# Kernel tuning notes

Measured on AMD Instinct MI355X. Metric: run time of the kernel, lower is better.

Reference implementation:

```python
import jax, jax.numpy as jnp
from jax import lax
import numpy as np

B, S, W = 32, 256, 16
WORD_VOCAB, WORD_DIM = 100000, 300
CHAR_VOCAB, CHAR_DIM = 101, 16  # len(char_vocab)+1
CH, WH = 16, 32                 # char_lstm_dim, lstm_size
GEN = 100
N_LABELS = 2


def _lstm(x, Wih, Whh, b, reverse=False):
    """Single-direction LSTM. x: [T, N, D]. Returns (outputs [T,N,H], final h [N,H]).
    Torch gate order: i, f, g, o."""
    pre = jnp.einsum('tnd,hd->tnh', x, Wih) + b  # [T, N, 4H]
    if reverse:
        pre = pre[::-1]
    H = Whh.shape[1]
    N = x.shape[1]

    def step(carry, xt):
        h, c = carry
        g = xt + h @ Whh.T
        i, f, gg, o = jnp.split(g, 4, axis=-1)
        c = jax.nn.sigmoid(f) * c + jax.nn.sigmoid(i) * jnp.tanh(gg)
        h = jax.nn.sigmoid(o) * jnp.tanh(c)
        return (h, c), h

    init = (jnp.zeros((N, H), x.dtype), jnp.zeros((N, H), x.dtype))
    (hT, _), hs = lax.scan(step, init, pre)
    if reverse:
        hs = hs[::-1]
    return hs, hT


def setup_inputs() -> dict:
    key = jax.random.key(0)
    ks = jax.random.split(key, 16)
    sc = lambda *shape: 0.1

    def rn(k, shape):
        return jax.random.normal(k, shape, dtype=jnp.float32) * 0.1

    return {
        'word_ids': jax.random.randint(ks[0], (B, S), 0, WORD_VOCAB),
        'char_ids': jax.random.randint(ks[1], (B, S, W), 0, CHAR_VOCAB),
        'word_table': rn(ks[2], (WORD_VOCAB, WORD_DIM)),
        'char_table': rn(ks[3], (CHAR_VOCAB, CHAR_DIM)),
        'c_Wih_f': rn(ks[4], (4 * CH, CHAR_DIM)), 'c_Whh_f': rn(ks[5], (4 * CH, CH)),
        'c_b_f': jnp.zeros((4 * CH,), jnp.float32),
        'c_Wih_b': rn(ks[6], (4 * CH, CHAR_DIM)), 'c_Whh_b': rn(ks[7], (4 * CH, CH)),
        'c_b_b': jnp.zeros((4 * CH,), jnp.float32),
        'gen_W': rn(ks[8], (GEN, WORD_DIM + 2 * CH)), 'gen_b': jnp.zeros((GEN,), jnp.float32),
        'w_Wih_f': rn(ks[9], (4 * WH, GEN)), 'w_Whh_f': rn(ks[10], (4 * WH, WH)),
        'w_b_f': jnp.zeros((4 * WH,), jnp.float32),
        'w_Wih_b': rn(ks[11], (4 * WH, GEN)), 'w_Whh_b': rn(ks[12], (4 * WH, WH)),
        'w_b_b': jnp.zeros((4 * WH,), jnp.float32),
        'out_W': rn(ks[13], (N_LABELS, 2 * WH)), 'out_b': jnp.zeros((N_LABELS,), jnp.float32),
    }


def reference(word_ids, char_ids, word_table, char_table,
              c_Wih_f, c_Whh_f, c_b_f, c_Wih_b, c_Whh_b, c_b_b,
              gen_W, gen_b,
              w_Wih_f, w_Whh_f, w_b_f, w_Wih_b, w_Whh_b, w_b_b,
              out_W, out_b):
    # Word embedding lookup: [B, S, WORD_DIM]
    word_e = word_table[word_ids]
    # Char embedding: [B, S, W, CHAR_DIM] -> char biLSTM over W, final states.
    char_e = char_table[char_ids].reshape(B * S, W, CHAR_DIM).transpose(1, 0, 2)  # [W, B*S, C]
    _, hf = _lstm(char_e, c_Wih_f, c_Whh_f, c_b_f, reverse=False)
    _, hb = _lstm(char_e, c_Wih_b, c_Whh_b, c_b_b, reverse=True)
    char_repr = jnp.concatenate([hf, hb], axis=-1).reshape(B, S, 2 * CH)
    # Concat word + char reprs, gen layer + gelu (dropout p=0 / eval).
    word_output = jnp.concatenate([word_e, char_repr], axis=-1)  # [B, S, 332]
    word_vecs = jax.nn.gelu(word_output @ gen_W.T + gen_b, approximate=False)  # [B, S, GEN]
    # Word-level biLSTM over S, per-step outputs.
    x = word_vecs.transpose(1, 0, 2)  # [S, B, GEN]
    of, _ = _lstm(x, w_Wih_f, w_Whh_f, w_b_f, reverse=False)
    ob, _ = _lstm(x, w_Wih_b, w_Whh_b, w_b_b, reverse=True)
    lstm_out = jnp.concatenate([of, ob], axis=-1).transpose(1, 0, 2)  # [B, S, 2*WH]
    # Output layer + sigmoid.
    return jax.nn.sigmoid(lstm_out @ out_W.T + out_b)  # [B, S, N_LABELS]
```

## Files before the change

### kernel.cpp

```cpp
#include <hip/hip_runtime.h>
#include <hip/hip_bf16.h>

#define B_    32
#define S_    256
#define BS_   8192
#define Wc_   16
#define CDIM_ 16
#define CH_   16
#define WDIM_ 300
#define KX_   332
#define XC_   336
#define GEN_  100
#define WVP_  104
#define WH_   32
#define NG_   128

constexpr size_t OFF_WV   = 0;
constexpr size_t OFF_PRE  = OFF_WV   + (size_t)BS_*WVP_;
constexpr size_t OFF_LO   = OFF_PRE  + (size_t)2*S_*B_*NG_;
constexpr size_t OFF_CHB  = OFF_LO   + (size_t)BS_*64;
constexpr size_t OFF_GWT  = OFF_CHB  + (size_t)BS_*32;
constexpr size_t OFF_WIHT = OFF_GWT  + (size_t)KX_*128;
constexpr size_t OFF_WHHT = OFF_WIHT + (size_t)2*GEN_*NG_;
constexpr size_t OFF_OW   = OFF_WHHT + (size_t)2*WH_*NG_;

__device__ __forceinline__ float sigm(float x){ return __builtin_amdgcn_rcpf(1.f + __expf(-x)); }
__device__ __forceinline__ float tanh_(float x){ return 1.f - 2.f*__builtin_amdgcn_rcpf(1.f + __expf(2.f*x)); }
__device__ __forceinline__ float rdlane(float v, int lane){
  return __uint_as_float(__builtin_amdgcn_readlane(__float_as_uint(v), lane));
}

__global__ void k_prep(const float* gen_W, const float* wih_f, const float* wih_b,
                       const float* whh_f, const float* whh_b, const float* out_W,
                       float* ws){
  int idx = blockIdx.x*blockDim.x + threadIdx.x;
  int stride = gridDim.x*blockDim.x;
  for (int i = idx; i < GEN_*KX_; i += stride){
    int j = i / KX_, k = i - j*KX_;
    ws[OFF_GWT + (size_t)k*128 + j] = gen_W[i];
  }
  for (int i = idx; i < NG_*GEN_; i += stride){
    int g = i / GEN_, k = i - g*GEN_;
    ws[OFF_WIHT + 0*GEN_*NG_ + (size_t)k*NG_ + g] = wih_f[i];
    ws[OFF_WIHT + 1*GEN_*NG_ + (size_t)k*NG_ + g] = wih_b[i];
  }
  for (int i = idx; i < NG_*WH_; i += stride){
    int g = i / WH_, k = i - g*WH_;
    ws[OFF_WHHT + 0*WH_*NG_ + (size_t)k*NG_ + g] = whh_f[i];
    ws[OFF_WHHT + 1*WH_*NG_ + (size_t)k*NG_ + g] = whh_b[i];
  }
  for (int i = idx; i < 2*64; i += stride) ws[OFF_OW + i] = out_W[i];
}

__global__ void __launch_bounds__(256, 2) k_char(const int* char_ids, const float* char_table,
                       const float* Wih_f, const float* Whh_f, const float* b_f,
                       const float* Wih_b, const float* Whh_b, const float* b_b,
                       float* ws){
  __shared__ float xr[16*324];
  const int dir = blockIdx.x & 1;
  const int sg  = blockIdx.x >> 1;
  const int tid = threadIdx.x;
  const float* WI = dir ? Wih_b : Wih_f;
  const float* WH = dir ? Whh_b : Whh_f;
  const float* BB = dir ? b_b  : b_f;
  const int ls = tid >> 4, u = tid & 15;
  const int seq0 = sg * 16;
  {
    const int id = char_ids[(seq0 + ls)*Wc_ + u];
    const float4* sr = (const float4*)(char_table + (size_t)id*CDIM_);
    float4 v0 = sr[0], v1 = sr[1], v2 = sr[2], v3 = sr[3];
    float* xw = &xr[ls*324 + u*20];
    *(float4*)(xw+0)  = v0; *(float4*)(xw+4)  = v1;
    *(float4*)(xw+8)  = v2; *(float4*)(xw+12) = v3;
  }
  float wi[4][16];
  #pragma unroll
  for (int g = 0; g < 4; ++g){
    const float4* wr = (const float4*)(WI + (size_t)(g*16+u)*CDIM_);
    float4 a = wr[0], b = wr[1], c = wr[2], d = wr[3];
    wi[g][0]=a.x; wi[g][1]=a.y; wi[g][2]=a.z; wi[g][3]=a.w;
    wi[g][4]=b.x; wi[g][5]=b.y; wi[g][6]=b.z; wi[g][7]=b.w;
    wi[g][8]=c.x; wi[g][9]=c.y; wi[g][10]=c.z; wi[g][11]=c.w;
    wi[g][12]=d.x; wi[g][13]=d.y; wi[g][14]=d.z; wi[g][15]=d.w;
  }
  float bias[4];
  #pragma unroll
  for (int g = 0; g < 4; ++g) bias[g] = BB[g*16+u];
  __syncthreads();
  float xp[16][4];
  const float* xb = &xr[ls*324];
  #pragma unroll
  for (int p = 0; p < 16; ++p){
    const int tm = dir ? (15-p) : p;
    const float4 x0 = *(const float4*)(xb + tm*20 + 0);
    const float4 x1 = *(const float4*)(xb + tm*20 + 4);
    const float4 x2 = *(const float4*)(xb + tm*20 + 8);
    const float4 x3 = *(const float4*)(xb + tm*20 + 12);
    float xk[16] = {x0.x,x0.y,x0.z,x0.w, x1.x,x1.y,x1.z,x1.w,
                    x2.x,x2.y,x2.z,x2.w, x3.x,x3.y,x3.z,x3.w};
    #pragma unroll
    for (int g = 0; g < 4; ++g){
      float a0 = bias[g], a1 = 0.f;
      #pragma unroll
      for (int k = 0; k < 16; k += 2){ a0 += wi[g][k]*xk[k]; a1 += wi[g][k+1]*xk[k+1]; }
      xp[p][g] = a0 + a1;
    }
  }
  float wh[4][16];
  #pragma unroll
  for (int g = 0; g < 4; ++g){
    const float4* wr = (const float4*)(WH + (size_t)(g*16+u)*CH_);
    float4 a = wr[0], b = wr[1], c = wr[2], d = wr[3];
    wh[g][0]=a.x; wh[g][1]=a.y; wh[g][2]=a.z; wh[g][3]=a.w;
    wh[g][4]=b.x; wh[g][5]=b.y; wh[g][6]=b.z; wh[g][7]=b.w;
    wh[g][8]=c.x; wh[g][9]=c.y; wh[g][10]=c.z; wh[g][11]=c.w;
    wh[g][12]=d.x; wh[g][13]=d.y; wh[g][14]=d.z; wh[g][15]=d.w;
  }
  const int lbase = (tid & 63) & 48;
  float h = 0.f, c = 0.f;
  #pragma unroll
  for (int p = 0; p < 16; ++p){
    float ai = xp[p][0], af = xp[p][1], ag = xp[p][2], ao = xp[p][3];
    #pragma unroll
    for (int k = 0; k < 16; ++k){
      const float hk = __shfl(h, lbase + k, 64);
      ai += wh[0][k]*hk; af += wh[1][k]*hk;
      ag += wh[2][k]*hk; ao += wh[3][k]*hk;
    }
    c = sigm(af)*c + sigm(ai)*tanh_(ag);
    h = sigm(ao)*tanh_(c);
  }
  ws[OFF_CHB + (size_t)(seq0 + ls)*32 + dir*16 + u] = h;
}

__global__ void k_gen(const int* word_ids, const float* word_table, const float* gen_b, float* ws){
  __shared__ __align__(16) float xt[16*XC_];
  __shared__ int wids[16];
  const int r0 = blockIdx.x*16;
  if (threadIdx.x < 16) wids[threadIdx.x] = word_ids[r0 + threadIdx.x];
  __syncthreads();
  float4* xt4 = (float4*)xt;
  for (int i = threadIdx.x; i < 16*75; i += 128){
    const int r = i/75, q = i - r*75;
    xt4[r*84 + q] = ((const float4*)(word_table + (size_t)wids[r]*WDIM_))[q];
  }
  for (int i = threadIdx.x; i < 16*8; i += 128){
    const int r = i >> 3, q = i & 7;
    xt4[r*84 + 75 + q] = ((const float4*)(ws + OFF_CHB + (size_t)(r0+r)*32))[q];
  }
  __syncthreads();
  const int j = threadIdx.x;
  const float bj = (j < GEN_) ? gen_b[j] : 0.f;
  float acc[16];
  #pragma unroll
  for (int r = 0; r < 16; ++r) acc[r] = bj;
  const float* WT = ws + OFF_GWT;
  for (int k4 = 0; k4 < KX_/4; ++k4){
    const int k = k4*4;
    const float w0 = WT[(size_t)(k+0)*128 + j];
    const float w1 = WT[(size_t)(k+1)*128 + j];
    const float w2 = WT[(size_t)(k+2)*128 + j];
    const float w3 = WT[(size_t)(k+3)*128 + j];
    #pragma unroll
    for (int r = 0; r < 16; ++r){
      const float4 xv = xt4[r*84 + k4];
      acc[r] += w0*xv.x + w1*xv.y + w2*xv.z + w3*xv.w;
    }
  }
  if (j < GEN_){
    float* wv = ws + OFF_WV;
    #pragma unroll
    for (int r = 0; r < 16; ++r){
      const float a = acc[r];
      wv[(size_t)(r0+r)*WVP_ + j] = 0.5f*a*(1.f + erff(a*0.70710678118f));
    }
  }
}

__global__ void k_wpre(const float* wb_f, const float* wb_b, float* ws){
  __shared__ __align__(16) float xt[8*WVP_];
  const int d  = blockIdx.x & 1;
  const int r0 = (blockIdx.x >> 1)*8;
  const float4* WVr = (const float4*)(ws + OFF_WV + (size_t)r0*WVP_);
  float4* xt4 = (float4*)xt;
  for (int i = threadIdx.x; i < 8*(WVP_/4); i += 128) xt4[i] = WVr[i];
  __syncthreads();
  const int g = threadIdx.x;
  const float wb = (d ? wb_b : wb_f)[g];
  float acc[8];
  #pragma unroll
  for (int r = 0; r < 8; ++r) acc[r] = wb;
  const float* WT = ws + OFF_WIHT + (size_t)d*GEN_*NG_;
  for (int k4 = 0; k4 < GEN_/4; ++k4){
    const int k = k4*4;
    const float w0 = WT[(size_t)(k+0)*NG_ + g];
    const float w1 = WT[(size_t)(k+1)*NG_ + g];
    const float w2 = WT[(size_t)(k+2)*NG_ + g];
    const float w3 = WT[(size_t)(k+3)*NG_ + g];
    #pragma unroll
    for (int r = 0; r < 8; ++r){
      const float4 xv = xt4[r*(WVP_/4) + k4];
      acc[r] += w0*xv.x + w1*xv.y + w2*xv.z + w3*xv.w;
    }
  }
  float* pre = ws + OFF_PRE + (size_t)d*S_*B_*NG_;
  #pragma unroll
  for (int r = 0; r < 8; ++r){
    const int row = r0 + r, b = row >> 8, s = row & 255;
    pre[((size_t)s*B_ + b)*NG_ + g] = acc[r];
  }
}

__global__ void __launch_bounds__(64) k_wlstm(float* ws){
  const int d = blockIdx.x >> 5;
  const int n = blockIdx.x & 31;
  const int l = threadIdx.x;
  const float* WT = ws + OFF_WHHT + (size_t)d*WH_*NG_;
  float wA[32], wB[32];
  #pragma unroll
  for (int k = 0; k < 32; ++k){ wA[k] = WT[(size_t)k*NG_ + l]; wB[k] = WT[(size_t)k*NG_ + 64 + l]; }
  const float* pre = ws + OFF_PRE + (size_t)d*S_*B_*NG_ + (size_t)n*NG_;
  float* lo = ws + OFF_LO;
  float cst = 0.f, h = 0.f;
  int tt = d ? (S_-1) : 0;
  const int stp = d ? -1 : 1;
  {
    const float* pr = pre + (size_t)tt*B_*NG_;
    h = 0.f;
    cst = 0.f;
  }
  float pA = pre[(size_t)tt*B_*NG_ + l];
  float pB = pre[(size_t)tt*B_*NG_ + 64 + l];
  for (int t = 0; t < S_; ++t){
    float pA2 = 0.f, pB2 = 0.f;
    if (t + 1 < S_){
      const float* prn = pre + (size_t)(tt+stp)*B_*NG_;
      pA2 = prn[l]; pB2 = prn[64 + l];
    }
    float aA0 = pA, aA1 = 0.f, aA2 = 0.f, aA3 = 0.f;
    float aB0 = pB, aB1 = 0.f, aB2 = 0.f, aB3 = 0.f;
    #pragma unroll
    for (int k = 0; k < 32; k += 4){
      const float h0 = rdlane(h, k+0);
      const float h1 = rdlane(h, k+1);
      const float h2 = rdlane(h, k+2);
      const float h3 = rdlane(h, k+3);
      aA0 += wA[k+0]*h0; aB0 += wB[k+0]*h0;
      aA1 += wA[k+1]*h1; aB1 += wB[k+1]*h1;
      aA2 += wA[k+2]*h2; aB2 += wB[k+2]*h2;
      aA3 += wA[k+3]*h3; aB3 += wB[k+3]*h3;
    }
    const float aA = (aA0+aA1)+(aA2+aA3);
    const float aB = (aB0+aB1)+(aB2+aB3);
    const float fga = __shfl_xor(aA, 32);
    const float oga = __shfl_xor(aB, 32);
    const float cc = sigm(fga)*cst + sigm(aA)*tanh_(aB);
    cst = cc;
    h = sigm(oga)*tanh_(cc);
    if (l < 32) lo[((size_t)n*S_ + tt)*64 + d*32 + l] = h;
    tt += stp; pA = pA2; pB = pB2;
  }
}

__global__ void k_out(const float* ws, const float* out_b, float* out){
  const int row = blockIdx.x*blockDim.x + threadIdx.x;
  const float4* lo = (const float4*)(ws + OFF_LO + (size_t)row*64);
  const float* OW = ws + OFF_OW;
  float a0 = out_b[0], a1 = out_b[1];
  #pragma unroll
  for (int q = 0; q < 16; ++q){
    const float4 v = lo[q];
    a0 += OW[q*4+0]*v.x + OW[q*4+1]*v.y + OW[q*4+2]*v.z + OW[q*4+3]*v.w;
    a1 += OW[64+q*4+0]*v.x + OW[64+q*4+1]*v.y + OW[64+q*4+2]*v.z + OW[64+q*4+3]*v.w;
  }
  out[row*2+0] = sigm(a0);
  out[row*2+1] = sigm(a1);
}

extern "C" void kernel_launch(void* const* d_in, const int* in_sizes, int n_in,
                              void* d_out, int out_size, void* d_ws, size_t ws_size,
                              hipStream_t stream){
  (void)in_sizes; (void)n_in; (void)out_size; (void)ws_size;
  const int*   word_ids   = (const int*)  d_in[0];
  const int*   char_ids   = (const int*)  d_in[1];
  const float* word_table = (const float*)d_in[2];
  const float* char_table = (const float*)d_in[3];
  const float* c_Wih_f    = (const float*)d_in[4];
  const float* c_Whh_f    = (const float*)d_in[5];
  const float* c_b_f      = (const float*)d_in[6];
  const float* c_Wih_b    = (const float*)d_in[7];
  const float* c_Whh_b    = (const float*)d_in[8];
  const float* c_b_b      = (const float*)d_in[9];
  const float* gen_W      = (const float*)d_in[10];
  const float* gen_b      = (const float*)d_in[11];
  const float* w_Wih_f    = (const float*)d_in[12];
  const float* w_Whh_f    = (const float*)d_in[13];
  const float* w_b_f      = (const float*)d_in[14];
  const float* w_Wih_b    = (const float*)d_in[15];
  const float* w_Whh_b    = (const float*)d_in[16];
  const float* w_b_b      = (const float*)d_in[17];
  const float* out_W      = (const float*)d_in[18];
  const float* out_b      = (const float*)d_in[19];
  float* ws  = (float*)d_ws;
  float* out = (float*)d_out;

  hipLaunchKernelGGL(k_prep,  dim3(64),   dim3(256), 0, stream,
                     gen_W, w_Wih_f, w_Wih_b, w_Whh_f, w_Whh_b, out_W, ws);
  hipLaunchKernelGGL(k_char,  dim3(1024), dim3(256), 0, stream,
                     char_ids, char_table, c_Wih_f, c_Whh_f, c_b_f,
                     c_Wih_b, c_Whh_b, c_b_b, ws);
  hipLaunchKernelGGL(k_gen,   dim3(512),  dim3(128), 0, stream, word_ids, word_table, gen_b, ws);
  hipLaunchKernelGGL(k_wpre,  dim3(2048), dim3(128), 0, stream, w_b_f, w_b_b, ws);
  hipLaunchKernelGGL(k_wlstm, dim3(64),   dim3(64),  0, stream, ws);
  hipLaunchKernelGGL(k_out,   dim3(64),   dim3(128), 0, stream, ws, out_b, out);
}
```

Before: 210.7 us.

## Fuse gen and input projection, run both LSTM directions per block with staged output

Merges the gen+GELU kernel with the word-LSTM input projection so word vectors stay in shared memory instead of round-tripping through global memory, removing one launch. The word LSTM now runs forward and backward directions interleaved in one 64-thread block (32 blocks instead of 64), giving two independent dependency chains per step to hide latency, prefetches two steps ahead, and buffers hidden states in LDS before writing them out in 32-step chunks. Activations use exp2 intrinsics directly. The cost is doubled register pressure (128 weight registers) and the recurrent kernel using half as many CUs.

After: 278.4 us. 32.1% more time.

```diff
diff --git a/kernel.cpp b/kernel.cpp
--- a/kernel.cpp
+++ b/kernel.cpp
@@ -24,8 +24,12 @@
 constexpr size_t OFF_WHHT = OFF_WIHT + (size_t)2*GEN_*NG_;
 constexpr size_t OFF_OW   = OFF_WHHT + (size_t)2*WH_*NG_;
 
-__device__ __forceinline__ float sigm(float x){ return __builtin_amdgcn_rcpf(1.f + __expf(-x)); }
-__device__ __forceinline__ float tanh_(float x){ return 1.f - 2.f*__builtin_amdgcn_rcpf(1.f + __expf(2.f*x)); }
+__device__ __forceinline__ float sigm(float x){
+  return __builtin_amdgcn_rcpf(1.f + __builtin_amdgcn_exp2f(-1.44269504089f*x));
+}
+__device__ __forceinline__ float tanh_(float x){
+  return 1.f - 2.f*__builtin_amdgcn_rcpf(1.f + __builtin_amdgcn_exp2f(2.88539008178f*x));
+}
 __device__ __forceinline__ float rdlane(float v, int lane){
   return __uint_as_float(__builtin_amdgcn_readlane(__float_as_uint(v), lane));
 }
@@ -133,8 +137,10 @@
   ws[OFF_CHB + (size_t)(seq0 + ls)*32 + dir*16 + u] = h;
 }
 
-__global__ void k_gen(const int* word_ids, const float* word_table, const float* gen_b, float* ws){
+__global__ void k_genp(const int* word_ids, const float* word_table, const float* gen_b,
+                       const float* wb_f, const float* wb_b, float* ws){
   __shared__ __align__(16) float xt[16*XC_];
+  __shared__ __align__(16) float wvs[16*WVP_];
   __shared__ int wids[16];
   const int r0 = blockIdx.x*16;
   if (threadIdx.x < 16) wids[threadIdx.x] = word_ids[r0 + threadIdx.x];
@@ -168,98 +174,123 @@
     }
   }
   if (j < GEN_){
-    float* wv = ws + OFF_WV;
     #pragma unroll
     for (int r = 0; r < 16; ++r){
       const float a = acc[r];
-      wv[(size_t)(r0+r)*WVP_ + j] = 0.5f*a*(1.f + erff(a*0.70710678118f));
-    }
-  }
-}
-
-__global__ void k_wpre(const float* wb_f, const float* wb_b, float* ws){
-  __shared__ __align__(16) float xt[8*WVP_];
-  const int d  = blockIdx.x & 1;
-  const int r0 = (blockIdx.x >> 1)*8;
-  const float4* WVr = (const float4*)(ws + OFF_WV + (size_t)r0*WVP_);
-  float4* xt4 = (float4*)xt;
-  for (int i = threadIdx.x; i < 8*(WVP_/4); i += 128) xt4[i] = WVr[i];
+      wvs[r*WVP_ + j] = 0.5f*a*(1.f + erff(a*0.70710678118f));
+    }
+  }
   __syncthreads();
   const int g = threadIdx.x;
-  const float wb = (d ? wb_b : wb_f)[g];
-  float acc[8];
-  #pragma unroll
-  for (int r = 0; r < 8; ++r) acc[r] = wb;
-  const float* WT = ws + OFF_WIHT + (size_t)d*GEN_*NG_;
-  for (int k4 = 0; k4 < GEN_/4; ++k4){
-    const int k = k4*4;
-    const float w0 = WT[(size_t)(k+0)*NG_ + g];
-    const float w1 = WT[(size_t)(k+1)*NG_ + g];
-    const float w2 = WT[(size_t)(k+2)*NG_ + g];
-    const float w3 = WT[(size_t)(k+3)*NG_ + g];
-    #pragma unroll
-    for (int r = 0; r < 8; ++r){
-      const float4 xv = xt4[r*(WVP_/4) + k4];
-      acc[r] += w0*xv.x + w1*xv.y + w2*xv.z + w3*xv.w;
-    }
-  }
-  float* pre = ws + OFF_PRE + (size_t)d*S_*B_*NG_;
-  #pragma unroll
-  for (int r = 0; r < 8; ++r){
-    const int row = r0 + r, b = row >> 8, s = row & 255;
-    pre[((size_t)s*B_ + b)*NG_ + g] = acc[r];
-  }
-}
-
-__global__ void __launch_bounds__(64) k_wlstm(float* ws){
-  const int d = blockIdx.x >> 5;
-  const int n = blockIdx.x & 31;
+  #pragma unroll
+  for (int d = 0; d < 2; ++d){
+    const float* W2 = ws + OFF_WIHT + (size_t)d*GEN_*NG_;
+    const float wb = (d ? wb_b : wb_f)[g];
+    float ac2[16];
+    #pragma unroll
+    for (int r = 0; r < 16; ++r) ac2[r] = wb;
+    for (int k4 = 0; k4 < GEN_/4; ++k4){
+      const int k = k4*4;
+      const float w0 = W2[(size_t)(k+0)*NG_ + g];
+      const float w1 = W2[(size_t)(k+1)*NG_ + g];
+      const float w2 = W2[(size_t)(k+2)*NG_ + g];
+      const float w3 = W2[(size_t)(k+3)*NG_ + g];
+      #pragma unroll
+      for (int r = 0; r < 16; ++r){
+        const float4 xv = *(const float4*)&wvs[r*WVP_ + k];
+        ac2[r] += w0*xv.x + w1*xv.y + w2*xv.z + w3*xv.w;
+      }
+    }
+    float* pre = ws + OFF_PRE + (size_t)d*S_*B_*NG_;
+    #pragma unroll
+    for (int r = 0; r < 16; ++r){
+      const int row = r0 + r, bb = row >> 8, ss = row & 255;
+      pre[((size_t)ss*B_ + bb)*NG_ + g] = ac2[r];
+    }
+  }
+}
+
+#define BN_ ((size_t)B_*NG_)
+__global__ void __launch_bounds__(64) k_wlstm(const float* __restrict__ WHT,
+                                              const float* __restrict__ PRE,
+                                              float* __restrict__ LO){
+  __shared__ __align__(16) float hring[5632];
+  const int n = blockIdx.x;
   const int l = threadIdx.x;
-  const float* WT = ws + OFF_WHHT + (size_t)d*WH_*NG_;
-  float wA[32], wB[32];
-  #pragma unroll
-  for (int k = 0; k < 32; ++k){ wA[k] = WT[(size_t)k*NG_ + l]; wB[k] = WT[(size_t)k*NG_ + 64 + l]; }
-  const float* pre = ws + OFF_PRE + (size_t)d*S_*B_*NG_ + (size_t)n*NG_;
-  float* lo = ws + OFF_LO;
-  float cst = 0.f, h = 0.f;
-  int tt = d ? (S_-1) : 0;
-  const int stp = d ? -1 : 1;
-  {
-    const float* pr = pre + (size_t)tt*B_*NG_;
-    h = 0.f;
-    cst = 0.f;
-  }
-  float pA = pre[(size_t)tt*B_*NG_ + l];
-  float pB = pre[(size_t)tt*B_*NG_ + 64 + l];
-  for (int t = 0; t < S_; ++t){
-    float pA2 = 0.f, pB2 = 0.f;
-    if (t + 1 < S_){
-      const float* prn = pre + (size_t)(tt+stp)*B_*NG_;
-      pA2 = prn[l]; pB2 = prn[64 + l];
-    }
-    float aA0 = pA, aA1 = 0.f, aA2 = 0.f, aA3 = 0.f;
-    float aB0 = pB, aB1 = 0.f, aB2 = 0.f, aB3 = 0.f;
-    #pragma unroll
-    for (int k = 0; k < 32; k += 4){
-      const float h0 = rdlane(h, k+0);
-      const float h1 = rdlane(h, k+1);
-      const float h2 = rdlane(h, k+2);
-      const float h3 = rdlane(h, k+3);
-      aA0 += wA[k+0]*h0; aB0 += wB[k+0]*h0;
-      aA1 += wA[k+1]*h1; aB1 += wB[k+1]*h1;
-      aA2 += wA[k+2]*h2; aB2 += wB[k+2]*h2;
-      aA3 += wA[k+3]*h3; aB3 += wB[k+3]*h3;
-    }
-    const float aA = (aA0+aA1)+(aA2+aA3);
-    const float aB = (aB0+aB1)+(aB2+aB3);
-    const float fga = __shfl_xor(aA, 32);
-    const float oga = __shfl_xor(aB, 32);
-    const float cc = sigm(fga)*cst + sigm(aA)*tanh_(aB);
-    cst = cc;
-    h = sigm(oga)*tanh_(cc);
-    if (l < 32) lo[((size_t)n*S_ + tt)*64 + d*32 + l] = h;
-    tt += stp; pA = pA2; pB = pB2;
-  }
+  float wAf[32], wBf[32], wAb[32], wBb[32];
+  #pragma unroll
+  for (int k = 0; k < 32; ++k){
+    wAf[k] = WHT[(size_t)k*NG_ + l];
+    wBf[k] = WHT[(size_t)k*NG_ + 64 + l];
+    wAb[k] = WHT[(size_t)(32 + k)*NG_ + l];
+    wBb[k] = WHT[(size_t)(32 + k)*NG_ + 64 + l];
+  }
+  const float* pf = PRE + (size_t)n*NG_;
+  const float* pb = PRE + (size_t)S_*BN_ + (size_t)n*NG_;
+  float cf = 0.f, hf = 0.f, cb = 0.f, hb = 0.f;
+
+  float f0A = pf[l],          f0B = pf[64+l];
+  float f1A = pf[BN_+l],      f1B = pf[BN_+64+l];
+  float b0A = pb[(size_t)(S_-1)*BN_ + l], b0B = pb[(size_t)(S_-1)*BN_ + 64+l];
+  float b1A = pb[(size_t)(S_-2)*BN_ + l], b1B = pb[(size_t)(S_-2)*BN_ + 64+l];
+
+#define WSTEP2(FA, FB, BA, BB, sidx) { \
+    float aAf0 = (FA), aAf1 = 0.f, aBf0 = (FB), aBf1 = 0.f; \
+    float aAb0 = (BA), aAb1 = 0.f, aBb0 = (BB), aBb1 = 0.f; \
+    _Pragma("unroll") \
+    for (int k = 0; k < 32; k += 2){ \
+      const float hf0 = rdlane(hf, k);   const float hf1 = rdlane(hf, k+1); \
+      const float hb0 = rdlane(hb, k);   const float hb1 = rdlane(hb, k+1); \
+      aAf0 += wAf[k]*hf0;   aBf0 += wBf[k]*hf0; \
+      aAf1 += wAf[k+1]*hf1; aBf1 += wBf[k+1]*hf1; \
+      aAb0 += wAb[k]*hb0;   aBb0 += wBb[k]*hb0; \
+      aAb1 += wAb[k+1]*hb1; aBb1 += wBb[k+1]*hb1; \
+    } \
+    const float aAf = aAf0 + aAf1, aBf = aBf0 + aBf1; \
+    const float aAb = aAb0 + aAb1, aBb = aBb0 + aBb1; \
+    const float fgf = __shfl_xor(aAf, 32), ogf = __shfl_xor(aBf, 32); \
+    const float fgb = __shfl_xor(aAb, 32), ogb = __shfl_xor(aBb, 32); \
+    cf = sigm(fgf)*cf + sigm(aAf)*tanh_(aBf); \
+    hf = sigm(ogf)*tanh_(cf); \
+    cb = sigm(fgb)*cb + sigm(aAb)*tanh_(aBb); \
+    hb = sigm(ogb)*tanh_(cb); \
+    if (l < 32){ \
+      hring[((sidx) & 31)*36 + l]        = hf; \
+      hring[1152 + ((sidx) & 31)*36 + l] = hb; \
+    } \
+  }
+
+  for (int s = 0; s < S_; s += 2){
+    float nf0A=0.f,nf0B=0.f,nf1A=0.f,nf1B=0.f,nb0A=0.f,nb0B=0.f,nb1A=0.f,nb1B=0.f;
+    if (s + 2 < S_){
+      nf0A = pf[(size_t)(s+2)*BN_ + l];   nf0B = pf[(size_t)(s+2)*BN_ + 64+l];
+      nf1A = pf[(size_t)(s+3)*BN_ + l];   nf1B = pf[(size_t)(s+3)*BN_ + 64+l];
+      nb0A = pb[(size_t)(S_-3-s)*BN_ + l]; nb0B = pb[(size_t)(S_-3-s)*BN_ + 64+l];
+      nb1A = pb[(size_t)(S_-4-s)*BN_ + l]; nb1B = pb[(size_t)(S_-4-s)*BN_ + 64+l];
+    }
+    WSTEP2(f0A, f0B, b0A, b0B, s)
+    WSTEP2(f1A, f1B, b1A, b1B, s+1)
+    f0A=nf0A; f0B=nf0B; f1A=nf1A; f1B=nf1B;
+    b0A=nb0A; b0B=nb0B; b1A=nb1A; b1B=nb1B;
+
+    if ((s & 31) == 30){
+      const int s0 = s & ~31;
+      const int srow = l >> 1, half = l & 1;
+      {
+        const int sf = s0 + srow;
+        const float4* src = (const float4*)&hring[srow*36 + half*16];
+        float4* dst = (float4*)(LO + ((size_t)n*S_ + sf)*64 + half*16);
+        dst[0]=src[0]; dst[1]=src[1]; dst[2]=src[2]; dst[3]=src[3];
+      }
+      {
+        const int tb = S_ - 1 - (s0 + srow);
+        const float4* src = (const float4*)&hring[1152 + srow*36 + half*16];
+        float4* dst = (float4*)(LO + ((size_t)n*S_ + tb)*64 + 32 + half*16);
+        dst[0]=src[0]; dst[1]=src[1]; dst[2]=src[2]; dst[3]=src[3];
+      }
+    }
+  }
+#undef WSTEP2
 }
 
 __global__ void k_out(const float* ws, const float* out_b, float* out){
@@ -309,8 +340,9 @@
   hipLaunchKernelGGL(k_char,  dim3(1024), dim3(256), 0, stream,
                      char_ids, char_table, c_Wih_f, c_Whh_f, c_b_f,
                      c_Wih_b, c_Whh_b, c_b_b, ws);
-  hipLaunchKernelGGL(k_gen,   dim3(512),  dim3(128), 0, stream, word_ids, word_table, gen_b, ws);
-  hipLaunchKernelGGL(k_wpre,  dim3(2048), dim3(128), 0, stream, w_b_f, w_b_b, ws);
-  hipLaunchKernelGGL(k_wlstm, dim3(64),   dim3(64),  0, stream, ws);
+  hipLaunchKernelGGL(k_genp,  dim3(512),  dim3(128), 0, stream,
+                     word_ids, word_table, gen_b, w_b_f, w_b_b, ws);
+  hipLaunchKernelGGL(k_wlstm, dim3(32),   dim3(64),  0, stream,
+                     ws + OFF_WHHT, ws + OFF_PRE, ws + OFF_LO);
   hipLaunchKernelGGL(k_out,   dim3(64),   dim3(128), 0, stream, ws, out_b, out);
 }
```
